# Performance work log

Hardware: AMD Instinct MI355X
Metric: run time of the kernel (lower is better)

## Reference

```python
import jax, jax.numpy as jnp
import numpy as np

B, H, S, DK = 1, 16, 4096, 64
SQRT_DK = float(DK) ** 0.5


def setup_inputs() -> dict:
    key = jax.random.key(0)
    kq, kk, kv = jax.random.split(key, 3)
    q = jax.random.normal(kq, (B, H, S, DK), dtype=jnp.float32)
    k = jax.random.normal(kk, (B, H, S, DK), dtype=jnp.float32)
    v = jax.random.normal(kv, (B, H, S, DK), dtype=jnp.float32)
    # causal mask: 1 where attention allowed, 0 where masked
    mask = jnp.tril(jnp.ones((S, S), dtype=jnp.int32))[None, None, :, :]
    return {"q": q, "k": k, "v": v, "mask": mask}


def reference(q, k, v, mask):
    # score = q @ k^T / sqrt(d_k)  -> [B, H, S, S]
    score = jnp.einsum("bhqd,bhkd->bhqk", q, k) / SQRT_DK
    # masked_fill(mask == 0, -inf)
    score = jnp.where(mask == 0, -jnp.inf, score)
    attn = jax.nn.softmax(score, axis=-1)
    # dropout with p=0.0 is identity
    return jnp.einsum("bhqk,bhkd->bhqd", attn, v)
```

## Files before the change

### kernel.cpp

```cpp
#include <hip/hip_runtime.h>

#define NH 16
#define SEQ 4096
#define DK 64
#define LSTR 72

typedef __fp16   fp16x2 __attribute__((ext_vector_type(2)));
typedef _Float16 f16x2 __attribute__((ext_vector_type(2)));
typedef _Float16 f16x4 __attribute__((ext_vector_type(4)));
typedef _Float16 f16x8 __attribute__((ext_vector_type(8)));
typedef float    f32x4 __attribute__((ext_vector_type(4)));

__device__ __forceinline__ f16x4 pk4(float a, float b, float c, float d) {
    f16x2 lo = __builtin_bit_cast(f16x2, (fp16x2)__builtin_amdgcn_cvt_pkrtz(a, b));
    f16x2 hi = __builtin_bit_cast(f16x2, (fp16x2)__builtin_amdgcn_cvt_pkrtz(c, d));
    f16x4 r; r[0]=lo[0]; r[1]=lo[1]; r[2]=hi[0]; r[3]=hi[1];
    return r;
}
__device__ __forceinline__ f16x8 pk8(float4 a, float4 b) {
    f16x4 lo = pk4(a.x, a.y, a.z, a.w);
    f16x4 hi = pk4(b.x, b.y, b.z, b.w);
    f16x8 r;
    r[0]=lo[0]; r[1]=lo[1]; r[2]=lo[2]; r[3]=lo[3];
    r[4]=hi[0]; r[5]=hi[1]; r[6]=hi[2]; r[7]=hi[3];
    return r;
}
__device__ __forceinline__ f16x4 lo4(f16x8 x){return __builtin_shufflevector(x,x,0,1,2,3);}
__device__ __forceinline__ f16x4 hi4(f16x8 x){return __builtin_shufflevector(x,x,4,5,6,7);}

__global__ __launch_bounds__(512, 4) void sdpa_flash_v11(
    const float* __restrict__ q, const float* __restrict__ k,
    const float* __restrict__ v, float* __restrict__ out)
{
    __shared__ _Float16 Ks[2][64 * LSTR];
    __shared__ _Float16 Vt[2][64 * LSTR];

    const int t    = threadIdx.x;
    const int wave = t >> 6;
    const int lane = t & 63;
    const int ln   = lane & 15;
    const int quad = lane >> 4;

    const int h    = blockIdx.x & (NH - 1);
    const int pair = blockIdx.x >> 4;
    const int qA0  = pair * 64;
    const int qB0  = (63 - pair) * 64;
    const int qw   = ((wave < 4) ? qA0 : qB0) + (wave & 3) * 16;

    const float SC = 0.125f * 1.44269504088896f;

    const float* qrow = q + ((size_t)h * SEQ + qw + ln) * DK;
    f16x8 qf[2];
#pragma unroll
    for (int kk = 0; kk < 2; ++kk) {
        float4 a = *(const float4*)(qrow + kk * 32 + quad * 8);
        float4 b = *(const float4*)(qrow + kk * 32 + quad * 8 + 4);
        qf[kk] = pk8(a, b);
    }

    f32x4 O[4];
#pragma unroll
    for (int i = 0; i < 4; ++i) O[i] = (f32x4){0.f, 0.f, 0.f, 0.f};
    float l = 0.f;

    const float4* kh4 = (const float4*)(k + (size_t)h * SEQ * DK);
    const float*  vhp = v + (size_t)h * SEQ * DK;

    const int skey = t >> 3, sc8 = t & 7;
    const int svd  = t & 63, svc = t >> 6;
    const int vq   = svc >> 1, vkh = svc & 1;
    const float* vbase0 = vhp + (size_t)(32 * vkh + vq * 4) * DK + svd;

    float4 kpa, kpb;
    float  vpre[8];
    {
        kpa = kh4[skey * 16 + sc8 * 2];
        kpb = kh4[skey * 16 + sc8 * 2 + 1];
#pragma unroll
        for (int j = 0; j < 4; ++j) {
            vpre[j]     = vbase0[j * DK];
            vpre[4 + j] = vbase0[(16 + j) * DK];
        }
    }

    int buf = 0;
    for (int k0 = 0; k0 <= qB0; k0 += 64) {
        *(f16x8*)&Ks[buf][skey * LSTR + sc8 * 8] = pk8(kpa, kpb);
        {
            f16x4 vlo = pk4(vpre[0], vpre[1], vpre[2], vpre[3]);
            f16x4 vhi = pk4(vpre[4], vpre[5], vpre[6], vpre[7]);
            f16x8 vv;
            vv[0]=vlo[0]; vv[1]=vlo[1]; vv[2]=vlo[2]; vv[3]=vlo[3];
            vv[4]=vhi[0]; vv[5]=vhi[1]; vv[6]=vhi[2]; vv[7]=vhi[3];
            *(f16x8*)&Vt[buf][svd * LSTR + svc * 8] = vv;
        }
        __syncthreads();

        if (k0 < qB0) {
            const int kn = k0 + 64;
            kpa = kh4[(kn + skey) * 16 + sc8 * 2];
            kpb = kh4[(kn + skey) * 16 + sc8 * 2 + 1];
            const float* vb = vbase0 + (size_t)kn * DK;
#pragma unroll
            for (int j = 0; j < 4; ++j) {
                vpre[j]     = vb[j * DK];
                vpre[4 + j] = vb[(16 + j) * DK];
            }
        }

        if (k0 <= qw + 15) {
            const bool diag = (k0 + 63 > qw);
            f16x4 pf[4];
#pragma unroll
            for (int ksub = 0; ksub < 4; ++ksub) {
                const _Float16* kr = &Ks[buf][(ksub * 16 + ln) * LSTR + quad * 8];
                f16x8 a0 = *(const f16x8*)kr;
                f16x8 a1 = *(const f16x8*)(kr + 32);
                f32x4 acc = (f32x4){0.f, 0.f, 0.f, 0.f};
                acc = __builtin_amdgcn_mfma_f32_16x16x32_f16(a0, qf[0], acc, 0, 0, 0);
                acc = __builtin_amdgcn_mfma_f32_16x16x32_f16(a1, qf[1], acc, 0, 0, 0);
                if (diag) {
                    const int keyb = k0 + ksub * 16 + quad * 4;
#pragma unroll
                    for (int r = 0; r < 4; ++r)
                        if (keyb + r > qw + ln) acc[r] = -1e30f;
                }
                float p0 = __builtin_amdgcn_exp2f(fmaf(acc[0], SC, -12.f));
                float p1 = __builtin_amdgcn_exp2f(fmaf(acc[1], SC, -12.f));
                float p2 = __builtin_amdgcn_exp2f(fmaf(acc[2], SC, -12.f));
                float p3 = __builtin_amdgcn_exp2f(fmaf(acc[3], SC, -12.f));
                l += (p0 + p1) + (p2 + p3);
                pf[ksub] = pk4(p0, p1, p2, p3);
            }
#pragma unroll
            for (int dsub = 0; dsub < 4; ++dsub) {
                const _Float16* vr = &Vt[buf][(dsub * 16 + ln) * LSTR + quad * 16];
                f16x8 v01 = *(const f16x8*)vr;
                f16x8 v23 = *(const f16x8*)(vr + 8);
                O[dsub] = __builtin_amdgcn_mfma_f32_16x16x16f16(lo4(v01), pf[0], O[dsub], 0, 0, 0);
                O[dsub] = __builtin_amdgcn_mfma_f32_16x16x16f16(hi4(v01), pf[1], O[dsub], 0, 0, 0);
                O[dsub] = __builtin_amdgcn_mfma_f32_16x16x16f16(lo4(v23), pf[2], O[dsub], 0, 0, 0);
                O[dsub] = __builtin_amdgcn_mfma_f32_16x16x16f16(hi4(v23), pf[3], O[dsub], 0, 0, 0);
            }
        }
        buf ^= 1;
    }

    l += __shfl_xor(l, 16);
    l += __shfl_xor(l, 32);
    const float inv = 1.f / l;
    float* op = out + ((size_t)h * SEQ + qw + ln) * DK + quad * 4;
#pragma unroll
    for (int dsub = 0; dsub < 4; ++dsub) {
        float4 r;
        r.x = O[dsub][0] * inv; r.y = O[dsub][1] * inv;
        r.z = O[dsub][2] * inv; r.w = O[dsub][3] * inv;
        *(float4*)(op + dsub * 16) = r;
    }
}

extern "C" void kernel_launch(void* const* d_in, const int* in_sizes, int n_in,
                              void* d_out, int out_size, void* d_ws, size_t ws_size,
                              hipStream_t stream) {
    const float* q = (const float*)d_in[0];
    const float* k = (const float*)d_in[1];
    const float* v = (const float*)d_in[2];
    float* out = (float*)d_out;

    dim3 grid(NH * 32);
    dim3 block(512);
    sdpa_flash_v11<<<grid, block, 0, stream>>>(q, k, v, out);
}
```

Measured before the change: 186.8 us.

## Replace paired causal q-blocks with one 64-row block per 256-thread workgroup

The kernel stops pairing a short and a long causal query block inside a 512-thread workgroup. Each 256-thread workgroup now handles a single 64-row query block, launched longest-first (reverse order) across twice as many workgroups. Each thread stages twice as much K/V per tile. This removes the idle waves that pairing caused, where the short half finished early but had to keep syncing through the long half's loop. The cost is losing explicit load balancing, which is now left to the hardware scheduler's longest-first ordering, plus more per-thread global loads and register use.

After: 195.2 us. +4.5%, slower.

```diff
diff --git a/kernel.cpp b/kernel.cpp
--- a/kernel.cpp
+++ b/kernel.cpp
@@ -28,7 +28,7 @@
 __device__ __forceinline__ f16x4 lo4(f16x8 x){return __builtin_shufflevector(x,x,0,1,2,3);}
 __device__ __forceinline__ f16x4 hi4(f16x8 x){return __builtin_shufflevector(x,x,4,5,6,7);}
 
-__global__ __launch_bounds__(512, 4) void sdpa_flash_v11(
+__global__ __launch_bounds__(256, 4) void sdpa_flash_v13(
     const float* __restrict__ q, const float* __restrict__ k,
     const float* __restrict__ v, float* __restrict__ out)
 {
@@ -42,10 +42,9 @@
     const int quad = lane >> 4;
 
     const int h    = blockIdx.x & (NH - 1);
-    const int pair = blockIdx.x >> 4;
-    const int qA0  = pair * 64;
-    const int qB0  = (63 - pair) * 64;
-    const int qw   = ((wave < 4) ? qA0 : qB0) + (wave & 3) * 16;
+    const int qidx = 63 - (blockIdx.x >> 4);
+    const int q0   = qidx * 64;
+    const int qw   = q0 + wave * 16;
 
     const float SC = 0.125f * 1.44269504088896f;
 
@@ -66,49 +65,65 @@
     const float4* kh4 = (const float4*)(k + (size_t)h * SEQ * DK);
     const float*  vhp = v + (size_t)h * SEQ * DK;
 
-    const int skey = t >> 3, sc8 = t & 7;
-    const int svd  = t & 63, svc = t >> 6;
-    const int vq   = svc >> 1, vkh = svc & 1;
-    const float* vbase0 = vhp + (size_t)(32 * vkh + vq * 4) * DK + svd;
+    const int skey = t >> 2, kc = t & 3;
+    const int svd = t & 63, c0 = t >> 6, c1 = c0 + 4;
+    const float* vbaseA = vhp + (size_t)(32 * (c0 & 1) + 4 * (c0 >> 1)) * DK + svd;
+    const float* vbaseB = vhp + (size_t)(32 * (c1 & 1) + 4 * (c1 >> 1)) * DK + svd;
 
-    float4 kpa, kpb;
-    float  vpre[8];
+    float4 kp0, kp1, kp2, kp3;
+    float  vpa[8], vpb[8];
     {
-        kpa = kh4[skey * 16 + sc8 * 2];
-        kpb = kh4[skey * 16 + sc8 * 2 + 1];
+        kp0 = kh4[skey * 16 + kc * 4];
+        kp1 = kh4[skey * 16 + kc * 4 + 1];
+        kp2 = kh4[skey * 16 + kc * 4 + 2];
+        kp3 = kh4[skey * 16 + kc * 4 + 3];
 #pragma unroll
         for (int j = 0; j < 4; ++j) {
-            vpre[j]     = vbase0[j * DK];
-            vpre[4 + j] = vbase0[(16 + j) * DK];
+            vpa[j]     = vbaseA[j * DK];
+            vpa[4 + j] = vbaseA[(16 + j) * DK];
+            vpb[j]     = vbaseB[j * DK];
+            vpb[4 + j] = vbaseB[(16 + j) * DK];
         }
     }
 
     int buf = 0;
-    for (int k0 = 0; k0 <= qB0; k0 += 64) {
-        *(f16x8*)&Ks[buf][skey * LSTR + sc8 * 8] = pk8(kpa, kpb);
+    for (int k0 = 0; k0 <= q0; k0 += 64) {
+        *(f16x8*)&Ks[buf][skey * LSTR + (2 * kc) * 8]     = pk8(kp0, kp1);
+        *(f16x8*)&Ks[buf][skey * LSTR + (2 * kc + 1) * 8] = pk8(kp2, kp3);
         {
-            f16x4 vlo = pk4(vpre[0], vpre[1], vpre[2], vpre[3]);
-            f16x4 vhi = pk4(vpre[4], vpre[5], vpre[6], vpre[7]);
-            f16x8 vv;
-            vv[0]=vlo[0]; vv[1]=vlo[1]; vv[2]=vlo[2]; vv[3]=vlo[3];
-            vv[4]=vhi[0]; vv[5]=vhi[1]; vv[6]=vhi[2]; vv[7]=vhi[3];
-            *(f16x8*)&Vt[buf][svd * LSTR + svc * 8] = vv;
+            f16x4 alo = pk4(vpa[0], vpa[1], vpa[2], vpa[3]);
+            f16x4 ahi = pk4(vpa[4], vpa[5], vpa[6], vpa[7]);
+            f16x8 av;
+            av[0]=alo[0]; av[1]=alo[1]; av[2]=alo[2]; av[3]=alo[3];
+            av[4]=ahi[0]; av[5]=ahi[1]; av[6]=ahi[2]; av[7]=ahi[3];
+            *(f16x8*)&Vt[buf][svd * LSTR + c0 * 8] = av;
+            f16x4 blo = pk4(vpb[0], vpb[1], vpb[2], vpb[3]);
+            f16x4 bhi = pk4(vpb[4], vpb[5], vpb[6], vpb[7]);
+            f16x8 bv;
+            bv[0]=blo[0]; bv[1]=blo[1]; bv[2]=blo[2]; bv[3]=blo[3];
+            bv[4]=bhi[0]; bv[5]=bhi[1]; bv[6]=bhi[2]; bv[7]=bhi[3];
+            *(f16x8*)&Vt[buf][svd * LSTR + c1 * 8] = bv;
         }
         __syncthreads();
 
-        if (k0 < qB0) {
+        if (k0 < q0) {
             const int kn = k0 + 64;
-            kpa = kh4[(kn + skey) * 16 + sc8 * 2];
-            kpb = kh4[(kn + skey) * 16 + sc8 * 2 + 1];
-            const float* vb = vbase0 + (size_t)kn * DK;
+            kp0 = kh4[(kn + skey) * 16 + kc * 4];
+            kp1 = kh4[(kn + skey) * 16 + kc * 4 + 1];
+            kp2 = kh4[(kn + skey) * 16 + kc * 4 + 2];
+            kp3 = kh4[(kn + skey) * 16 + kc * 4 + 3];
+            const float* vbA = vbaseA + (size_t)kn * DK;
+            const float* vbB = vbaseB + (size_t)kn * DK;
 #pragma unroll
             for (int j = 0; j < 4; ++j) {
-                vpre[j]     = vb[j * DK];
-                vpre[4 + j] = vb[(16 + j) * DK];
+                vpa[j]     = vbA[j * DK];
+                vpa[4 + j] = vbA[(16 + j) * DK];
+                vpb[j]     = vbB[j * DK];
+                vpb[4 + j] = vbB[(16 + j) * DK];
             }
         }
 
-        if (k0 <= qw + 15) {
+        {
             const bool diag = (k0 + 63 > qw);
             f16x4 pf[4];
 #pragma unroll
@@ -167,7 +182,7 @@
     const float* v = (const float*)d_in[2];
     float* out = (float*)d_out;
 
-    dim3 grid(NH * 32);
-    dim3 block(512);
-    sdpa_flash_v11<<<grid, block, 0, stream>>>(q, k, v, out);
+    dim3 grid(NH * 64);
+    dim3 block(256);
+    sdpa_flash_v13<<<grid, block, 0, stream>>>(q, k, v, out);
 }
```

## Load K fragments directly from global per wave instead of staging in LDS

Applied to the files above, without the earlier changes.

Removes the shared-memory K tile. Each wave now loads its K MFMA fragments straight from global memory as float4s, converting to fp16 in registers, and skips the load for key blocks it will not use. The goal is to cut LDS writes and reads and shrink LDS footprint. The cost is that the eight waves of a block each reread the same K tile through the cache, and the K loads are no longer prefetched a step ahead, so latency sits right before the MFMAs. The launch-bounds occupancy hint is also dropped.

Measured after the change: 441.8 us. 136% more time.

```diff
diff --git a/kernel.cpp b/kernel.cpp
--- a/kernel.cpp
+++ b/kernel.cpp
@@ -28,11 +28,10 @@
 __device__ __forceinline__ f16x4 lo4(f16x8 x){return __builtin_shufflevector(x,x,0,1,2,3);}
 __device__ __forceinline__ f16x4 hi4(f16x8 x){return __builtin_shufflevector(x,x,4,5,6,7);}
 
-__global__ __launch_bounds__(512, 4) void sdpa_flash_v11(
+__global__ __launch_bounds__(512) void sdpa_flash_v20(
     const float* __restrict__ q, const float* __restrict__ k,
     const float* __restrict__ v, float* __restrict__ out)
 {
-    __shared__ _Float16 Ks[2][64 * LSTR];
     __shared__ _Float16 Vt[2][64 * LSTR];
 
     const int t    = threadIdx.x;
@@ -63,29 +62,39 @@
     for (int i = 0; i < 4; ++i) O[i] = (f32x4){0.f, 0.f, 0.f, 0.f};
     float l = 0.f;
 
-    const float4* kh4 = (const float4*)(k + (size_t)h * SEQ * DK);
-    const float*  vhp = v + (size_t)h * SEQ * DK;
+    const float* khp = k + (size_t)h * SEQ * DK;
+    const float* vhp = v + (size_t)h * SEQ * DK;
 
-    const int skey = t >> 3, sc8 = t & 7;
     const int svd  = t & 63, svc = t >> 6;
     const int vq   = svc >> 1, vkh = svc & 1;
     const float* vbase0 = vhp + (size_t)(32 * vkh + vq * 4) * DK + svd;
 
-    float4 kpa, kpb;
-    float  vpre[8];
-    {
-        kpa = kh4[skey * 16 + sc8 * 2];
-        kpb = kh4[skey * 16 + sc8 * 2 + 1];
+    const float* kfb = khp + (size_t)ln * DK + quad * 8;
+
+    float vpre[8];
 #pragma unroll
-        for (int j = 0; j < 4; ++j) {
-            vpre[j]     = vbase0[j * DK];
-            vpre[4 + j] = vbase0[(16 + j) * DK];
-        }
+    for (int j = 0; j < 4; ++j) {
+        vpre[j]     = vbase0[j * DK];
+        vpre[4 + j] = vbase0[(16 + j) * DK];
     }
 
     int buf = 0;
     for (int k0 = 0; k0 <= qB0; k0 += 64) {
-        *(f16x8*)&Ks[buf][skey * LSTR + sc8 * 8] = pk8(kpa, kpb);
+        const bool act = (k0 <= qw + 15);
+
+        float4 kr0[4], kr1[4], kr2[4], kr3[4];
+        if (act) {
+            const float* kb = kfb + (size_t)k0 * DK;
+#pragma unroll
+            for (int ks = 0; ks < 4; ++ks) {
+                const float* kp = kb + (size_t)ks * 16 * DK;
+                kr0[ks] = *(const float4*)(kp);
+                kr1[ks] = *(const float4*)(kp + 4);
+                kr2[ks] = *(const float4*)(kp + 32);
+                kr3[ks] = *(const float4*)(kp + 36);
+            }
+        }
+
         {
             f16x4 vlo = pk4(vpre[0], vpre[1], vpre[2], vpre[3]);
             f16x4 vhi = pk4(vpre[4], vpre[5], vpre[6], vpre[7]);
@@ -97,10 +106,7 @@
         __syncthreads();
 
         if (k0 < qB0) {
-            const int kn = k0 + 64;
-            kpa = kh4[(kn + skey) * 16 + sc8 * 2];
-            kpb = kh4[(kn + skey) * 16 + sc8 * 2 + 1];
-            const float* vb = vbase0 + (size_t)kn * DK;
+            const float* vb = vbase0 + (size_t)(k0 + 64) * DK;
 #pragma unroll
             for (int j = 0; j < 4; ++j) {
                 vpre[j]     = vb[j * DK];
@@ -108,14 +114,13 @@
             }
         }
 
-        if (k0 <= qw + 15) {
+        if (act) {
             const bool diag = (k0 + 63 > qw);
             f16x4 pf[4];
 #pragma unroll
             for (int ksub = 0; ksub < 4; ++ksub) {
-                const _Float16* kr = &Ks[buf][(ksub * 16 + ln) * LSTR + quad * 8];
-                f16x8 a0 = *(const f16x8*)kr;
-                f16x8 a1 = *(const f16x8*)(kr + 32);
+                f16x8 a0 = pk8(kr0[ksub], kr1[ksub]);
+                f16x8 a1 = pk8(kr2[ksub], kr3[ksub]);
                 f32x4 acc = (f32x4){0.f, 0.f, 0.f, 0.f};
                 acc = __builtin_amdgcn_mfma_f32_16x16x32_f16(a0, qf[0], acc, 0, 0, 0);
                 acc = __builtin_amdgcn_mfma_f32_16x16x32_f16(a1, qf[1], acc, 0, 0, 0);
@@ -169,5 +174,5 @@
 
     dim3 grid(NH * 32);
     dim3 block(512);
-    sdpa_flash_v11<<<grid, block, 0, stream>>>(q, k, v, out);
+    sdpa_flash_v20<<<grid, block, 0, stream>>>(q, k, v, out);
 }
```
